# Performance work log

Hardware: AMD Instinct MI355X
Metric: run time of the kernel (lower is better)

The kernel has to match this reference:

```python
import jax, jax.numpy as jnp
import numpy as np

N_NODES = 50000
N_EDGES = 1250000
D_FEAT = 64


def setup_inputs() -> dict:
    key = jax.random.key(0)
    k1, k2, k3, k4 = jax.random.split(key, 4)
    feat = jax.random.normal(k1, (N_NODES, D_FEAT), dtype=jnp.float32)
    edge_weight = jax.random.uniform(k2, (N_EDGES,), dtype=jnp.float32)
    edge_src = jax.random.randint(k3, (N_EDGES,), 0, N_NODES, dtype=jnp.int64)
    edge_dst = jnp.sort(jax.random.randint(k4, (N_EDGES,), 0, N_NODES, dtype=jnp.int64))
    return {"feat": feat, "edge_weight": edge_weight,
            "edge_src": edge_src, "edge_dst": edge_dst}


def reference(feat, edge_weight, edge_src, edge_dst):
    # u_mul_e: gather source node features, scale by per-edge weight
    msgs = feat[edge_src] * edge_weight[:, None]          # [E, d]
    # fn.sum: scatter-add messages to destination nodes
    rst = jax.ops.segment_sum(msgs, edge_dst, num_segments=N_NODES)  # [N, d]
    return rst
```

## Files before the change

kernel.cpp:

```cpp
#include <hip/hip_runtime.h>

#define D_FEAT 64

__global__ __launch_bounds__(256) void build_rowptr_kernel(
    const int* __restrict__ edge_dst, int* __restrict__ rp,
    int n_edges, int n_nodes) {
  const int v = blockIdx.x * blockDim.x + threadIdx.x;
  if (v > n_nodes) return;
  int lo = 0, hi = n_edges;
  while (lo < hi) {
    const int mid = (lo + hi) >> 1;
    if (edge_dst[mid] < v) lo = mid + 1; else hi = mid;
  }
  rp[v] = lo;
}

__global__ __launch_bounds__(256) void gcn_gather_kernel(
    const float* __restrict__ feat,
    const float* __restrict__ edge_weight,
    const int* __restrict__ edge_src,
    const int* __restrict__ rp,
    float* __restrict__ out, int n_nodes) {
  const int wave = (blockIdx.x * blockDim.x + threadIdx.x) >> 6;
  const int lane = threadIdx.x & 63;
  if (wave >= n_nodes) return;

  const int e0 = rp[wave];
  const int e1 = rp[wave + 1];

  float acc0 = 0.0f, acc1 = 0.0f;

  for (int base = e0; base < e1; base += 64) {
    const int n = min(64, e1 - base);
    int   s = 0;
    float w = 0.0f;
    if (lane < n) {
      s = edge_src[base + lane];
      w = edge_weight[base + lane];
    }
    int i = 0;
    for (; i + 1 < n; i += 2) {
      const int   s0 = __shfl(s, i);
      const int   s1 = __shfl(s, i + 1);
      const float w0 = __shfl(w, i);
      const float w1 = __shfl(w, i + 1);
      acc0 = fmaf(feat[(size_t)s0 * D_FEAT + lane], w0, acc0);
      acc1 = fmaf(feat[(size_t)s1 * D_FEAT + lane], w1, acc1);
    }
    if (i < n) {
      const int   s0 = __shfl(s, i);
      const float w0 = __shfl(w, i);
      acc0 = fmaf(feat[(size_t)s0 * D_FEAT + lane], w0, acc0);
    }
  }
  out[(size_t)wave * D_FEAT + lane] = acc0 + acc1;
}

extern "C" void kernel_launch(void* const* d_in, const int* in_sizes, int n_in,
                              void* d_out, int out_size, void* d_ws, size_t ws_size,
                              hipStream_t stream) {
  const float* feat        = (const float*)d_in[0];
  const float* edge_weight = (const float*)d_in[1];
  const int*   edge_src    = (const int*)d_in[2];
  const int*   edge_dst    = (const int*)d_in[3];
  float* out = (float*)d_out;

  const int n_edges = in_sizes[1];
  const int n_nodes = out_size / D_FEAT;

  int* rp = (int*)d_ws;

  const int bp_threads = n_nodes + 1;
  build_rowptr_kernel<<<(bp_threads + 255) / 256, 256, 0, stream>>>(
      edge_dst, rp, n_edges, n_nodes);

  const int total_threads = n_nodes * 64;
  gcn_gather_kernel<<<(total_threads + 255) / 256, 256, 0, stream>>>(
      feat, edge_weight, edge_src, rp, out, n_nodes);
}
```

Measured before the change: 127.2 us.

## Vectorize gather with float4 across 16-lane subgroups; build rowptr via edge scatter

```diff
diff --git a/kernel.cpp b/kernel.cpp
--- a/kernel.cpp
+++ b/kernel.cpp
@@ -2,58 +2,80 @@
 
 #define D_FEAT 64
 
-__global__ __launch_bounds__(256) void build_rowptr_kernel(
+__global__ __launch_bounds__(256) void build_rowptr_scatter(
     const int* __restrict__ edge_dst, int* __restrict__ rp,
     int n_edges, int n_nodes) {
-  const int v = blockIdx.x * blockDim.x + threadIdx.x;
-  if (v > n_nodes) return;
-  int lo = 0, hi = n_edges;
-  while (lo < hi) {
-    const int mid = (lo + hi) >> 1;
-    if (edge_dst[mid] < v) lo = mid + 1; else hi = mid;
-  }
-  rp[v] = lo;
+  const int e = blockIdx.x * blockDim.x + threadIdx.x;
+  if (e > n_edges) return;
+  const int d0 = (e == 0) ? -1 : edge_dst[e - 1];
+  const int d1 = (e == n_edges) ? n_nodes : edge_dst[e];
+  for (int v = d0 + 1; v <= d1; ++v) rp[v] = e;
 }
 
-__global__ __launch_bounds__(256) void gcn_gather_kernel(
+__global__ __launch_bounds__(256) void gcn_gather4(
     const float* __restrict__ feat,
-    const float* __restrict__ edge_weight,
-    const int* __restrict__ edge_src,
+    const float* __restrict__ ew,
+    const int* __restrict__ esrc,
     const int* __restrict__ rp,
     float* __restrict__ out, int n_nodes) {
   const int wave = (blockIdx.x * blockDim.x + threadIdx.x) >> 6;
   const int lane = threadIdx.x & 63;
   if (wave >= n_nodes) return;
+  const int sub = lane >> 4;
+  const int fl  = lane & 15;
 
   const int e0 = rp[wave];
   const int e1 = rp[wave + 1];
 
-  float acc0 = 0.0f, acc1 = 0.0f;
+  float4 acc0 = {0.f, 0.f, 0.f, 0.f};
+  float4 acc1 = {0.f, 0.f, 0.f, 0.f};
+
+  const float4* feat4 = (const float4*)feat;
 
   for (int base = e0; base < e1; base += 64) {
     const int n = min(64, e1 - base);
     int   s = 0;
     float w = 0.0f;
     if (lane < n) {
-      s = edge_src[base + lane];
-      w = edge_weight[base + lane];
+      s = esrc[base + lane];
+      w = ew[base + lane];
     }
-    int i = 0;
-    for (; i + 1 < n; i += 2) {
-      const int   s0 = __shfl(s, i);
-      const int   s1 = __shfl(s, i + 1);
-      const float w0 = __shfl(w, i);
-      const float w1 = __shfl(w, i + 1);
-      acc0 = fmaf(feat[(size_t)s0 * D_FEAT + lane], w0, acc0);
-      acc1 = fmaf(feat[(size_t)s1 * D_FEAT + lane], w1, acc1);
-    }
-    if (i < n) {
-      const int   s0 = __shfl(s, i);
-      const float w0 = __shfl(w, i);
-      acc0 = fmaf(feat[(size_t)s0 * D_FEAT + lane], w0, acc0);
+    for (int i = 0; i < n; i += 8) {
+      const int   sA = __shfl(s, i + sub);
+      const float wA = __shfl(w, i + sub);
+      const int   sB = __shfl(s, i + 4 + sub);
+      const float wB = __shfl(w, i + 4 + sub);
+      const float4 rA = feat4[(size_t)sA * 16 + fl];
+      const float4 rB = feat4[(size_t)sB * 16 + fl];
+      acc0.x = fmaf(rA.x, wA, acc0.x);
+      acc0.y = fmaf(rA.y, wA, acc0.y);
+      acc0.z = fmaf(rA.z, wA, acc0.z);
+      acc0.w = fmaf(rA.w, wA, acc0.w);
+      acc1.x = fmaf(rB.x, wB, acc1.x);
+      acc1.y = fmaf(rB.y, wB, acc1.y);
+      acc1.z = fmaf(rB.z, wB, acc1.z);
+      acc1.w = fmaf(rB.w, wB, acc1.w);
     }
   }
-  out[(size_t)wave * D_FEAT + lane] = acc0 + acc1;
+
+  float4 acc;
+  acc.x = acc0.x + acc1.x;
+  acc.y = acc0.y + acc1.y;
+  acc.z = acc0.z + acc1.z;
+  acc.w = acc0.w + acc1.w;
+
+  acc.x += __shfl_xor(acc.x, 16);
+  acc.y += __shfl_xor(acc.y, 16);
+  acc.z += __shfl_xor(acc.z, 16);
+  acc.w += __shfl_xor(acc.w, 16);
+  acc.x += __shfl_xor(acc.x, 32);
+  acc.y += __shfl_xor(acc.y, 32);
+  acc.z += __shfl_xor(acc.z, 32);
+  acc.w += __shfl_xor(acc.w, 32);
+
+  if (lane < 16) {
+    ((float4*)(out + (size_t)wave * D_FEAT))[fl] = acc;
+  }
 }
 
 extern "C" void kernel_launch(void* const* d_in, const int* in_sizes, int n_in,
@@ -70,11 +92,11 @@
 
   int* rp = (int*)d_ws;
 
-  const int bp_threads = n_nodes + 1;
-  build_rowptr_kernel<<<(bp_threads + 255) / 256, 256, 0, stream>>>(
+  const int bp_threads = n_edges + 1;
+  build_rowptr_scatter<<<(bp_threads + 255) / 256, 256, 0, stream>>>(
       edge_dst, rp, n_edges, n_nodes);
 
   const int total_threads = n_nodes * 64;
-  gcn_gather_kernel<<<(total_threads + 255) / 256, 256, 0, stream>>>(
+  gcn_gather4<<<(total_threads + 255) / 256, 256, 0, stream>>>(
       feat, edge_weight, edge_src, rp, out, n_nodes);
 }
```

New measurement: 113.6 us. 1.12x faster.
